# Kernel tuning notes

Hardware: AMD Instinct MI355X
Metric: run time of the kernel (lower is better)

## Reference

```python
import jax, jax.numpy as jnp
import numpy as np

N_PTS = 1_000_000
B = 2048          # number of graphs
C_IN = 8
C_OUT = 32        # `channel` trivial irreps -> conv/activation width
WIDTH = 4.0       # kernel radial width
N_RINGS = 2
EPS = 1e-6


def setup_inputs() -> dict:
    key = jax.random.key(0)
    k = jax.random.split(key, 6)
    x = jax.random.normal(k[0], (N_PTS, C_IN), dtype=jnp.float32)
    coords = jax.random.normal(k[1], (N_PTS, 3), dtype=jnp.float32)
    batch = jnp.sort(jax.random.randint(k[2], (N_PTS,), 0, B))
    # steerable kernel weights: [C_out, C_in, n_rings * n_angular(=4: Y0 + Y1)]
    W = jax.random.normal(k[3], (C_OUT, C_IN, N_RINGS * 4), dtype=jnp.float32) * 0.1
    gamma = jnp.ones((C_OUT,), dtype=jnp.float32)
    beta = jnp.zeros((C_OUT,), dtype=jnp.float32)
    act_bias = jax.random.uniform(k[4], (C_OUT,), dtype=jnp.float32)
    return {"x": x, "coords": coords, "batch": batch, "W": W,
            "gamma": gamma, "beta": beta, "act_bias": act_bias}


def reference(x, coords, batch, W, gamma, beta, act_bias):
    n = x.shape[0]
    # --- global_mean_pool of coords per graph -> out_coords [B,3] ---
    cnt = jax.ops.segment_sum(jnp.ones((n,), x.dtype), batch, num_segments=B)
    cnt = jnp.maximum(cnt, 1.0)
    pos = jax.ops.segment_sum(coords, batch, num_segments=B) / cnt[:, None]
    # --- per-edge relative position: edge i = (point i -> center of graph batch[i]) ---
    rel = pos[batch] - coords                    # [N,3] gather (irregular access)
    d = jnp.linalg.norm(rel, axis=-1)            # [N]
    # --- radial Gaussian ring profile ---
    rings = jnp.linspace(0.0, WIDTH, N_RINGS)
    sigma = WIDTH / max(N_RINGS - 1, 1)
    radial = jnp.exp(-0.5 * ((d[:, None] - rings[None, :]) / sigma) ** 2)   # [N,R]
    # --- angular part: real spherical harmonics l=0 (const) and l=1 (direction) ---
    direc = rel / jnp.maximum(d, EPS)[:, None]
    ang = jnp.concatenate([jnp.ones((n, 1), x.dtype), direc], axis=-1)      # [N,4]
    basis = (radial[:, :, None] * ang[:, None, :]).reshape(n, -1)           # [N, R*4]
    # --- continuous-kernel point conv: per-edge kernel eval + message ---
    msg = jnp.einsum('eb,oib,ei->eo', basis, W, x)                          # [N,C_out]
    # --- scatter-add aggregation to graph centers ---
    out = jax.ops.segment_sum(msg, batch, num_segments=B)                   # [B,C_out]
    # --- IID batch norm (per-channel, batch statistics) ---
    mu = out.mean(axis=0)
    var = out.var(axis=0)
    out = (out - mu) / jnp.sqrt(var + 1e-5) * gamma + beta
    # --- NormNonLinearity (trivial fields) followed by NormPool: relu(|x| - b) ---
    y = jax.nn.relu(jnp.abs(out) - act_bias)                                # [B,C_out]
    return y
```

## Files before the change

kernel.cpp:

```cpp
#include <hip/hip_runtime.h>


#define RS16_STAGE(M, HALF)                                 \
  {                                                         \
    const bool hi_ = (lane & (M)) != 0;                     \
    _Pragma("unroll")                                       \
    for (int k = 0; k < (HALF); ++k) {                      \
      float send = hi_ ? acc[k] : acc[(HALF) + k];          \
      float keep = hi_ ? acc[(HALF) + k] : acc[k];          \
      acc[k] = keep + __shfl_xor(send, (M), 64);            \
    }                                                       \
  }

#define NBLK_STATS 64

__device__ __forceinline__ int rev4(int s) {
  return ((s & 1) << 3) | ((s & 2) << 1) | ((s & 4) >> 1) | ((s & 8) >> 3);
}

__device__ __forceinline__ void basis8(float rx, float ry, float rz,
                                       float* bas) {
  float d2 = rx * rx + ry * ry + rz * rz;
  float d = sqrtf(d2);
  float r0 = __expf(-0.03125f * d2);
  float tt = (d - 4.0f) * 0.25f;
  float r1 = __expf(-0.5f * tt * tt);
  float idm = 1.0f / fmaxf(d, 1e-6f);
  float ax = rx * idm, ay = ry * idm, az = rz * idm;
  bas[0] = r0; bas[1] = r0 * ax; bas[2] = r0 * ay; bas[3] = r0 * az;
  bas[4] = r1; bas[5] = r1 * ax; bas[6] = r1 * ay; bas[7] = r1 * az;
}

__device__ __forceinline__ int lower_bound64(const int* __restrict__ a,
                                             int n, int key, int lane) {
  int lo = 0, len = n;
  while (len > 64) {
    int chunk = (len + 63) >> 6;
    int p = lo + lane * chunk;
    bool c = (p < lo + len) && (a[p] < key);
    unsigned long long mask = __ballot(c);
    int m = __popcll(mask);
    if (m == 0) { len = 0; break; }
    int nlo = lo + (m - 1) * chunk + 1;
    int nhi = min(lo + m * chunk, lo + len);
    lo = nlo;
    len = nhi - nlo;
  }
  if (len > 0) {
    int p = lo + lane;
    bool c = (lane < len) && (a[p] < key);
    lo += __popcll(__ballot(c));
  }
  return lo;
}

__global__ __launch_bounds__(256) void graph_kernel(
    const float* __restrict__ x, const float* __restrict__ coords,
    const int* __restrict__ batch, const float* __restrict__ W,
    float* __restrict__ out_raw, int n) {
  __shared__ __align__(16) float pv[4][64][20];
  __shared__ float sredm[4][3];
  __shared__ float sred[4][64];
  __shared__ float sVg[64];
  __shared__ float pre2[4][32];
  __shared__ float smean[3];
  __shared__ int sbound[2];

  const int g = blockIdx.x;
  const int t = threadIdx.x;
  const int lane = t & 63;
  const int wv = t >> 6;

  if (wv < 2) {
    int r = lower_bound64(batch, n, g + wv, lane);
    if (lane == 0) sbound[wv] = r;
  }
  __syncthreads();
  const int lo = sbound[0], hi = sbound[1];
  const int cnt = hi - lo;

  float s1 = 0.f, s2 = 0.f, s3 = 0.f;
  for (int i = lo + t; i < hi; i += 256) {
    s1 += coords[(size_t)i * 3 + 0];
    s2 += coords[(size_t)i * 3 + 1];
    s3 += coords[(size_t)i * 3 + 2];
  }
#pragma unroll
  for (int m = 1; m < 64; m <<= 1) {
    s1 += __shfl_xor(s1, m, 64);
    s2 += __shfl_xor(s2, m, 64);
    s3 += __shfl_xor(s3, m, 64);
  }
  if (lane == 0) { sredm[wv][0] = s1; sredm[wv][1] = s2; sredm[wv][2] = s3; }
  __syncthreads();
  if (t < 3) {
    smean[t] = (sredm[0][t] + sredm[1][t] + sredm[2][t] + sredm[3][t]) /
               (float)max(cnt, 1);
  }
  __syncthreads();
  const float mx = smean[0], my = smean[1], mz = smean[2];

  const int q2 = lane >> 4;
  const int sub = lane & 15;
  float acc[16];
#pragma unroll
  for (int b = 0; b < 16; ++b) acc[b] = 0.f;

  const int niter = (cnt + 255) >> 8;
  for (int it = 0; it < niter; ++it) {
    const int ip = lo + it * 256 + wv * 64 + lane;
    const bool vp = ip < hi;
    const int ic = min(ip, n - 1);
    float cx = coords[(size_t)ic * 3 + 0];
    float cy = coords[(size_t)ic * 3 + 1];
    float cz = coords[(size_t)ic * 3 + 2];
    float bas[8];
    basis8(mx - cx, my - cy, mz - cz, bas);
    float4 xa = ((const float4*)x)[2 * (size_t)ic];
    float4 xb = ((const float4*)x)[2 * (size_t)ic + 1];
    if (!vp) {
      xa = make_float4(0.f, 0.f, 0.f, 0.f);
      xb = make_float4(0.f, 0.f, 0.f, 0.f);
    }
    float* dst = &pv[wv][lane][0];
    ((float4*)dst)[0] = xa;
    ((float4*)dst)[1] = xb;
    ((float4*)dst)[2] = make_float4(bas[0], bas[1], bas[2], bas[3]);
    ((float4*)dst)[3] = make_float4(bas[4], bas[5], bas[6], bas[7]);
#pragma unroll
    for (int j = 0; j < 4; ++j) {
      const float* src = &pv[wv][16 * j + sub][0];
      float2 xp = *(const float2*)(src + 2 * q2);
      float4 b03 = *(const float4*)(src + 8);
      float4 b47 = *(const float4*)(src + 12);
      acc[0]  += xp.x * b03.x;  acc[1]  += xp.x * b03.y;
      acc[2]  += xp.x * b03.z;  acc[3]  += xp.x * b03.w;
      acc[4]  += xp.x * b47.x;  acc[5]  += xp.x * b47.y;
      acc[6]  += xp.x * b47.z;  acc[7]  += xp.x * b47.w;
      acc[8]  += xp.y * b03.x;  acc[9]  += xp.y * b03.y;
      acc[10] += xp.y * b03.z;  acc[11] += xp.y * b03.w;
      acc[12] += xp.y * b47.x;  acc[13] += xp.y * b47.y;
      acc[14] += xp.y * b47.z;  acc[15] += xp.y * b47.w;
    }
  }

  RS16_STAGE(1, 8)
  RS16_STAGE(2, 4)
  RS16_STAGE(4, 2)
  RS16_STAGE(8, 1)
  sred[wv][16 * q2 + rev4(sub)] = acc[0];
  __syncthreads();
  if (t < 64) sVg[t] = sred[0][t] + sred[1][t] + sred[2][t] + sred[3][t];
  __syncthreads();

  const int o = t & 31;
  const int part = t >> 5;
  const float* wrow = W + (size_t)o * 64 + part * 8;
  float4 w0 = *(const float4*)(wrow);
  float4 w1 = *(const float4*)(wrow + 4);
  float4 v0 = *(const float4*)(&sVg[part * 8]);
  float4 v1 = *(const float4*)(&sVg[part * 8 + 4]);
  float r = w0.x * v0.x + w0.y * v0.y + w0.z * v0.z + w0.w * v0.w +
            w1.x * v1.x + w1.y * v1.y + w1.z * v1.z + w1.w * v1.w;
  r += __shfl_xor(r, 32, 64);
  if (lane < 32) pre2[wv][o] = r;
  __syncthreads();
  if (t < 32) {
    out_raw[(size_t)g * 32 + t] =
        pre2[0][t] + pre2[1][t] + pre2[2][t] + pre2[3][t];
  }
}

__global__ __launch_bounds__(256) void stats_kernel(
    const float* __restrict__ out_raw, float* __restrict__ spart, int B) {
  __shared__ float red[4][32], redq[4][32];
  const int t = threadIdx.x;
  const int o = t & 31;
  const int lane = t & 63;
  const int wv = t >> 6;
  const int stride = NBLK_STATS * 256;
  float s = 0.f, q = 0.f;
  for (int e = blockIdx.x * 256 + t; e < B * 32; e += stride) {
    float val = out_raw[e];
    s += val;
    q += val * val;
  }
  s += __shfl_xor(s, 32, 64);
  q += __shfl_xor(q, 32, 64);
  if (lane < 32) { red[wv][o] = s; redq[wv][o] = q; }
  __syncthreads();
  if (t < 32) {
    spart[blockIdx.x * 64 + t] =
        red[0][t] + red[1][t] + red[2][t] + red[3][t];
    spart[blockIdx.x * 64 + 32 + t] =
        redq[0][t] + redq[1][t] + redq[2][t] + redq[3][t];
  }
}

__global__ __launch_bounds__(256) void final_kernel(
    const float* __restrict__ out_raw, const float* __restrict__ spart,
    const float* __restrict__ gamma, const float* __restrict__ beta,
    const float* __restrict__ act_bias, float* __restrict__ out, int B) {
  __shared__ float sfold[4][64];
  __shared__ float sscale[32], sshift[32], sbias[32];
  const int t = threadIdx.x;
  const int total = B * 32;

  {
    const int slot = t & 63;
    const int grp = t >> 6;
    float s = 0.f;
#pragma unroll
    for (int b = 0; b < 16; ++b)
      s += spart[(grp * 16 + b) * 64 + slot];
    sfold[grp][slot] = s;
  }
  __syncthreads();
  if (t < 32) {
    float ssum = sfold[0][t] + sfold[1][t] + sfold[2][t] + sfold[3][t];
    float ssq  = sfold[0][32 + t] + sfold[1][32 + t] +
                 sfold[2][32 + t] + sfold[3][32 + t];
    float invB = 1.0f / (float)B;
    float mu = ssum * invB;
    float var = ssq * invB - mu * mu;
    float sc = rsqrtf(var + 1e-5f) * gamma[t];
    sscale[t] = sc;
    sshift[t] = beta[t] - mu * sc;
    sbias[t]  = act_bias[t];
  }
  __syncthreads();

  const int base = (blockIdx.x * 256 + t) * 4;
  if (base < total) {
    float4 vv = *(const float4*)(out_raw + base);
    const int o0 = base & 31;
    float r0 = fabsf(vv.x * sscale[o0 + 0] + sshift[o0 + 0]) - sbias[o0 + 0];
    float r1 = fabsf(vv.y * sscale[o0 + 1] + sshift[o0 + 1]) - sbias[o0 + 1];
    float r2 = fabsf(vv.z * sscale[o0 + 2] + sshift[o0 + 2]) - sbias[o0 + 2];
    float r3 = fabsf(vv.w * sscale[o0 + 3] + sshift[o0 + 3]) - sbias[o0 + 3];
    *(float4*)(out + base) = make_float4(fmaxf(r0, 0.f), fmaxf(r1, 0.f),
                                         fmaxf(r2, 0.f), fmaxf(r3, 0.f));
  }
}

extern "C" void kernel_launch(void* const* d_in, const int* in_sizes, int n_in,
                              void* d_out, int out_size, void* d_ws, size_t ws_size,
                              hipStream_t stream) {
  const float* x      = (const float*)d_in[0];
  const float* coords = (const float*)d_in[1];
  const int*   batch  = (const int*)d_in[2];
  const float* W      = (const float*)d_in[3];
  const float* gamma  = (const float*)d_in[4];
  const float* beta   = (const float*)d_in[5];
  const float* abias  = (const float*)d_in[6];
  float* out = (float*)d_out;

  int n = in_sizes[2];
  int B = out_size / 32;

  float* out_raw = (float*)d_ws;
  float* spart   = out_raw + (size_t)B * 32;

  graph_kernel<<<B, 256, 0, stream>>>(x, coords, batch, W, out_raw, n);
  stats_kernel<<<NBLK_STATS, 256, 0, stream>>>(out_raw, spart, B);
  int nblk_final = (B * 32 + 1023) / 1024;
  final_kernel<<<nblk_final, 256, 0, stream>>>(out_raw, spart, gamma, beta, abias, out, B);
}
```

Baseline: 26.65 us.

## Preload first 512 points into registers and reuse them across mean and conv passes

Each thread loads the coords and x of its first two points up front. Those values are used both for the per-graph coordinate mean and for the first two accumulation iterations, so they are not re-read from global memory in the second pass. This removes a second read of most of the data (about 488 points per graph) and issues the x loads early so they overlap the mean reduction. In exchange it raises register pressure and duplicates the accumulation body in code.

```diff
diff --git a/kernel.cpp b/kernel.cpp
--- a/kernel.cpp
+++ b/kernel.cpp
@@ -79,8 +79,25 @@
   const int lo = sbound[0], hi = sbound[1];
   const int cnt = hi - lo;
 
-  float s1 = 0.f, s2 = 0.f, s3 = 0.f;
-  for (int i = lo + t; i < hi; i += 256) {
+  const bool vA = t < cnt;
+  const bool vB = 256 + t < cnt;
+  const int iA = min(lo + t, n - 1);
+  const int iB = min(lo + 256 + t, n - 1);
+  float cAx = coords[(size_t)iA * 3 + 0];
+  float cAy = coords[(size_t)iA * 3 + 1];
+  float cAz = coords[(size_t)iA * 3 + 2];
+  float cBx = coords[(size_t)iB * 3 + 0];
+  float cBy = coords[(size_t)iB * 3 + 1];
+  float cBz = coords[(size_t)iB * 3 + 2];
+  float4 xA0 = ((const float4*)x)[2 * (size_t)iA];
+  float4 xA1 = ((const float4*)x)[2 * (size_t)iA + 1];
+  float4 xB0 = ((const float4*)x)[2 * (size_t)iB];
+  float4 xB1 = ((const float4*)x)[2 * (size_t)iB + 1];
+
+  float s1 = (vA ? cAx : 0.f) + (vB ? cBx : 0.f);
+  float s2 = (vA ? cAy : 0.f) + (vB ? cBy : 0.f);
+  float s3 = (vA ? cAz : 0.f) + (vB ? cBz : 0.f);
+  for (int i = lo + 512 + t; i < hi; i += 256) {
     s1 += coords[(size_t)i * 3 + 0];
     s2 += coords[(size_t)i * 3 + 1];
     s3 += coords[(size_t)i * 3 + 2];
@@ -106,8 +123,64 @@
 #pragma unroll
   for (int b = 0; b < 16; ++b) acc[b] = 0.f;
 
+  {
+    float bas[8];
+    basis8(mx - cAx, my - cAy, mz - cAz, bas);
+    if (!vA) {
+      xA0 = make_float4(0.f, 0.f, 0.f, 0.f);
+      xA1 = make_float4(0.f, 0.f, 0.f, 0.f);
+    }
+    float* dst = &pv[wv][lane][0];
+    ((float4*)dst)[0] = xA0;
+    ((float4*)dst)[1] = xA1;
+    ((float4*)dst)[2] = make_float4(bas[0], bas[1], bas[2], bas[3]);
+    ((float4*)dst)[3] = make_float4(bas[4], bas[5], bas[6], bas[7]);
+#pragma unroll
+    for (int j = 0; j < 4; ++j) {
+      const float* src = &pv[wv][16 * j + sub][0];
+      float2 xp = *(const float2*)(src + 2 * q2);
+      float4 b03 = *(const float4*)(src + 8);
+      float4 b47 = *(const float4*)(src + 12);
+      acc[0]  += xp.x * b03.x;  acc[1]  += xp.x * b03.y;
+      acc[2]  += xp.x * b03.z;  acc[3]  += xp.x * b03.w;
+      acc[4]  += xp.x * b47.x;  acc[5]  += xp.x * b47.y;
+      acc[6]  += xp.x * b47.z;  acc[7]  += xp.x * b47.w;
+      acc[8]  += xp.y * b03.x;  acc[9]  += xp.y * b03.y;
+      acc[10] += xp.y * b03.z;  acc[11] += xp.y * b03.w;
+      acc[12] += xp.y * b47.x;  acc[13] += xp.y * b47.y;
+      acc[14] += xp.y * b47.z;  acc[15] += xp.y * b47.w;
+    }
+  }
+  if (cnt > 256) {
+    float bas[8];
+    basis8(mx - cBx, my - cBy, mz - cBz, bas);
+    if (!vB) {
+      xB0 = make_float4(0.f, 0.f, 0.f, 0.f);
+      xB1 = make_float4(0.f, 0.f, 0.f, 0.f);
+    }
+    float* dst = &pv[wv][lane][0];
+    ((float4*)dst)[0] = xB0;
+    ((float4*)dst)[1] = xB1;
+    ((float4*)dst)[2] = make_float4(bas[0], bas[1], bas[2], bas[3]);
+    ((float4*)dst)[3] = make_float4(bas[4], bas[5], bas[6], bas[7]);
+#pragma unroll
+    for (int j = 0; j < 4; ++j) {
+      const float* src = &pv[wv][16 * j + sub][0];
+      float2 xp = *(const float2*)(src + 2 * q2);
+      float4 b03 = *(const float4*)(src + 8);
+      float4 b47 = *(const float4*)(src + 12);
+      acc[0]  += xp.x * b03.x;  acc[1]  += xp.x * b03.y;
+      acc[2]  += xp.x * b03.z;  acc[3]  += xp.x * b03.w;
+      acc[4]  += xp.x * b47.x;  acc[5]  += xp.x * b47.y;
+      acc[6]  += xp.x * b47.z;  acc[7]  += xp.x * b47.w;
+      acc[8]  += xp.y * b03.x;  acc[9]  += xp.y * b03.y;
+      acc[10] += xp.y * b03.z;  acc[11] += xp.y * b03.w;
+      acc[12] += xp.y * b47.x;  acc[13] += xp.y * b47.y;
+      acc[14] += xp.y * b47.z;  acc[15] += xp.y * b47.w;
+    }
+  }
   const int niter = (cnt + 255) >> 8;
-  for (int it = 0; it < niter; ++it) {
+  for (int it = 2; it < niter; ++it) {
     const int ip = lo + it * 256 + wv * 64 + lane;
     const bool vp = ip < hi;
     const int ic = min(ip, n - 1);
```

Result: faster. 25.13 us, median of 2 (-5.7%).
